# Performance work log

Hardware: AMD Instinct MI355X
Metric: run time of the kernel (lower is better)

## Reference

```python
import jax, jax.numpy as jnp
import numpy as np

B_SZ, L, D_INNER = 2, 1024, 2048
D_STATE, DT_RANK = 16, 64


def setup_inputs() -> dict:
    key = jax.random.key(0)
    k1, k2, k3, k4 = jax.random.split(key, 4)
    x = jax.random.normal(k1, (B_SZ, L, D_INNER), dtype=jnp.float32)
    # Linear weights: torch layout (out_features, in_features); scaled ~1/sqrt(fan_in)
    W_x = jax.random.normal(k2, (DT_RANK + 2 * D_STATE, D_INNER), dtype=jnp.float32) / np.sqrt(D_INNER)
    W_dt = jax.random.normal(k3, (D_INNER, DT_RANK), dtype=jnp.float32) / np.sqrt(DT_RANK)
    b_dt = jax.random.normal(k4, (D_INNER,), dtype=jnp.float32) * 0.1
    # A_log = log(arange(1, d_state+1)) broadcast to (d_inner, d_state), as in __init__
    A_log = jnp.broadcast_to(jnp.log(jnp.arange(1, D_STATE + 1, dtype=jnp.float32)), (D_INNER, D_STATE))
    D = jnp.ones((D_INNER,), dtype=jnp.float32)
    return {"x": x, "W_x": W_x, "W_dt": W_dt, "b_dt": b_dt, "A_log": A_log, "D": D}


def reference(x, W_x, W_dt, b_dt, A_log, D):
    # x: (B, L, d_inner)
    xz = jnp.einsum('bld,kd->blk', x, W_x)                       # (B, L, dt_rank + 2*d_state)
    delta_raw = xz[..., :DT_RANK]
    B_in = xz[..., DT_RANK:DT_RANK + D_STATE]                    # (B, L, d_state)
    C_in = xz[..., DT_RANK + D_STATE:]                           # (B, L, d_state)
    delta = jax.nn.softplus(jnp.einsum('blr,dr->bld', delta_raw, W_dt) + b_dt)  # (B, L, d_inner)
    A = -jnp.exp(A_log)                                          # (d_inner, d_state), negative
    A_bar = jnp.exp(delta[..., None] * A)                        # (B, L, d_inner, d_state)
    B_bar = delta[..., None] * B_in[:, :, None, :]               # (B, L, d_inner, d_state)

    def step(h, inputs):
        A_t, Bx_t, C_t = inputs                                  # (B,d,n), (B,d,n), (B,n)
        h = A_t * h + Bx_t
        y_t = jnp.sum(h * C_t[:, None, :], axis=-1)              # (B, d_inner)
        return h, y_t

    h0 = jnp.zeros((x.shape[0], D_INNER, D_STATE), dtype=x.dtype)
    Bx = B_bar * x[..., None]                                    # (B, L, d_inner, d_state)
    # scan over L: move L to leading axis
    _, ys = jax.lax.scan(step, h0, (jnp.moveaxis(A_bar, 1, 0), jnp.moveaxis(Bx, 1, 0), jnp.moveaxis(C_in, 1, 0)))
    y = jnp.moveaxis(ys, 0, 1) + D * x                           # (B, L, d_inner)
    return y
```

## Files before the change

kernel.cpp:

```cpp
#include <hip/hip_runtime.h>
#include <hip/hip_bf16.h>

#define B_SZ 2
#define LSEQ 1024
#define DIN  2048
#define DST  16
#define DTR  64
#define KTOT 96
#define NROW (B_SZ * LSEQ)
#define NCH  64
#define TCH  16
#define KSP  32

__device__ __forceinline__ float b2f(unsigned int u) {
    union { unsigned int i; float f; } v;
    v.i = (u & 0xffffu) << 16;
    return v.f;
}

__device__ __forceinline__ float ldf(const void* p, size_t i, bool f32) {
    return f32 ? ((const float*)p)[i] : b2f(((const unsigned short*)p)[i]);
}

__device__ __forceinline__ float4 ld4(const void* p, size_t i, bool f32) {
    if (f32) return *(const float4*)((const float*)p + i);
    const uint2 u = *(const uint2*)((const unsigned short*)p + i);
    float4 v;
    v.x = b2f(u.x); v.y = b2f(u.x >> 16);
    v.z = b2f(u.y); v.w = b2f(u.y >> 16);
    return v;
}

__device__ __forceinline__ float softplus_f(float v) {
    return (v > 20.f) ? v : log1pf(__expf(v));
}

__global__ __launch_bounds__(256) void k_detect(const void* __restrict__ x,
                                                int* __restrict__ flag) {
    __shared__ int cnt;
    if (threadIdx.x == 0) cnt = 0;
    __syncthreads();
    const unsigned short* u = (const unsigned short*)x;
    int my = 0;
    for (int i = threadIdx.x; i < 4096; i += 256) {
        unsigned short v = u[2 * i];
        float af = fabsf(b2f(v));
        if (v == 0 || (af >= 6.0e-8f && af <= 1.7e7f)) my++;
    }
    atomicAdd(&cnt, my);
    __syncthreads();
    if (threadIdx.x == 0) *flag = (cnt < 2048) ? 1 : 0;
}

__global__ __launch_bounds__(256, 4) void k_proj(
    const void* __restrict__ x,
    const void* __restrict__ Wx,
    const int*  __restrict__ flag,
    float* __restrict__ part)
{
    const bool f32 = (*flag != 0);
    __shared__ float lx[32][68];
    __shared__ float lw[32][100];
    const int tid = threadIdx.x;
    const int bx = blockIdx.x;
    const int by = blockIdx.y;
    const int rt = tid >> 4, ct = tid & 15;
    const int r0 = rt * 4, c0 = ct * 6;

    float acc[4][6];
    #pragma unroll
    for (int i = 0; i < 4; i++)
        #pragma unroll
        for (int k = 0; k < 6; k++) acc[i][k] = 0.f;

    for (int half = 0; half < 2; half++) {
        const int k0 = by * 64 + half * 32;
        #pragma unroll
        for (int it = 0; it < 2; it++) {
            const int idx = tid + it * 256;
            const int r = idx >> 3, q = idx & 7;
            float4 v = ld4(x, (size_t)(bx * 64 + r) * DIN + k0 + q * 4, f32);
            lx[q * 4 + 0][r] = v.x; lx[q * 4 + 1][r] = v.y;
            lx[q * 4 + 2][r] = v.z; lx[q * 4 + 3][r] = v.w;
        }
        #pragma unroll
        for (int it = 0; it < 3; it++) {
            const int idx = tid + it * 256;
            const int c = idx >> 3, q = idx & 7;
            float4 v = ld4(Wx, (size_t)c * DIN + k0 + q * 4, f32);
            lw[q * 4 + 0][c] = v.x; lw[q * 4 + 1][c] = v.y;
            lw[q * 4 + 2][c] = v.z; lw[q * 4 + 3][c] = v.w;
        }
        __syncthreads();

        #pragma unroll 4
        for (int j = 0; j < 32; j++) {
            const float4 xa = *(const float4*)&lx[j][r0];
            const float2 w0 = *(const float2*)&lw[j][c0];
            const float2 w1 = *(const float2*)&lw[j][c0 + 2];
            const float2 w2 = *(const float2*)&lw[j][c0 + 4];
            const float xr[4] = {xa.x, xa.y, xa.z, xa.w};
            const float wc[6] = {w0.x, w0.y, w1.x, w1.y, w2.x, w2.y};
            #pragma unroll
            for (int i = 0; i < 4; i++)
                #pragma unroll
                for (int k = 0; k < 6; k++)
                    acc[i][k] += xr[i] * wc[k];
        }
        __syncthreads();
    }

    float* p = part + ((size_t)by * NROW + bx * 64 + r0) * KTOT + c0;
    #pragma unroll
    for (int i = 0; i < 4; i++) {
        float* row = p + (size_t)i * KTOT;
        *(float2*)(row)     = make_float2(acc[i][0], acc[i][1]);
        *(float2*)(row + 2) = make_float2(acc[i][2], acc[i][3]);
        *(float2*)(row + 4) = make_float2(acc[i][4], acc[i][5]);
    }
}

__global__ __launch_bounds__(256, 4) void k_comb(
    const float* __restrict__ part,
    float* __restrict__ drw, float* __restrict__ Bin, float* __restrict__ Cin)
{
    const int idx = blockIdx.x * 256 + threadIdx.x;
    float s = 0.f;
    #pragma unroll 8
    for (int ks = 0; ks < KSP; ks++)
        s += part[(size_t)ks * NROW * KTOT + idx];
    const int r = idx / KTOT, c = idx % KTOT;
    if (c < DTR)            drw[r * DTR + c] = s;
    else if (c < DTR + DST) Bin[r * DST + (c - DTR)] = s;
    else                    Cin[r * DST + (c - DTR - DST)] = s;
}

__global__ __launch_bounds__(256, 2) void k_scan1(
    const void* __restrict__ x,
    const float* __restrict__ drw,
    const float* __restrict__ Bin,
    const void* __restrict__ Wdt,
    const void* __restrict__ bdt,
    const void* __restrict__ Alog,
    const int*  __restrict__ flag,
    float* __restrict__ Pb,
    float* __restrict__ Hb)
{
    const bool f32 = (*flag != 0);
    __shared__ float x_lds[TCH][256];
    __shared__ float dt_lds[TCH][256];
    __shared__ float drw_lds[TCH][DTR];
    __shared__ float Bs[TCH * DST];
    const int tid = threadIdx.x;
    const int d = blockIdx.x * 256 + tid;
    const int c = blockIdx.y;
    const int b = blockIdx.z;
    const int row0 = b * LSEQ + c * TCH;

    #pragma unroll
    for (int it = 0; it < 4; it++) {
        const int f4 = tid + it * 256;
        const int t  = f4 >> 6, q4 = f4 & 63;
        float4 v = ld4(x, (size_t)(row0 + t) * DIN + blockIdx.x * 256 + q4 * 4, f32);
        *(float4*)&x_lds[t][q4 * 4] = v;
    }
    #pragma unroll
    for (int it = 0; it < 4; it++) {
        const int f = tid + it * 256;
        const int r = f >> 6, k = f & 63;
        drw_lds[r][k] = drw[(size_t)(row0 + r) * DTR + k];
    }
    Bs[tid] = Bin[(size_t)row0 * DST + tid];

    float A[DST];
    #pragma unroll
    for (int sq = 0; sq < DST / 4; sq++) {
        float4 av = ld4(Alog, (size_t)d * DST + sq * 4, f32);
        A[sq * 4 + 0] = -__expf(av.x); A[sq * 4 + 1] = -__expf(av.y);
        A[sq * 4 + 2] = -__expf(av.z); A[sq * 4 + 3] = -__expf(av.w);
    }
    __syncthreads();

    {
        float dtv[TCH];
        const float bd = ldf(bdt, (size_t)d, f32);
        #pragma unroll
        for (int r = 0; r < TCH; r++) dtv[r] = bd;
        #pragma unroll 4
        for (int kq = 0; kq < DTR / 4; kq++) {
            const float4 w = ld4(Wdt, (size_t)d * DTR + kq * 4, f32);
            #pragma unroll
            for (int r = 0; r < TCH; r++) {
                const float4 a = *(const float4*)&drw_lds[r][kq * 4];
                dtv[r] += a.x * w.x; dtv[r] += a.y * w.y;
                dtv[r] += a.z * w.z; dtv[r] += a.w * w.w;
            }
        }
        #pragma unroll
        for (int r = 0; r < TCH; r++) dt_lds[r][tid] = softplus_f(dtv[r]);
    }

    float P[DST], H[DST];
    #pragma unroll
    for (int s = 0; s < DST; s++) { P[s] = 1.f; H[s] = 0.f; }

    #pragma unroll 1
    for (int t = 0; t < TCH; t++) {
        const float dtv_t = dt_lds[t][tid];
        const float xv    = x_lds[t][tid];
        const float u     = dtv_t * xv;
        const float* bs = Bs + t * DST;
        #pragma unroll
        for (int s = 0; s < DST; s++) {
            const float e = __expf(dtv_t * A[s]);
            P[s] *= e;
            H[s] = e * H[s] + u * bs[s];
        }
    }

    const size_t base = (size_t)(b * NCH + c) * DST * DIN + d;
    #pragma unroll
    for (int s = 0; s < DST; s++) {
        Pb[base + (size_t)s * DIN] = P[s];
        Hb[base + (size_t)s * DIN] = H[s];
    }
}

__global__ __launch_bounds__(256, 4) void k_scan2(
    const float* __restrict__ Pb,
    const float* __restrict__ Hb,
    float* __restrict__ hin)
{
    const int idx = blockIdx.x * 256 + threadIdx.x;
    const int b   = idx / (DST * DIN);
    const int rem = idx % (DST * DIN);
    float h = 0.f;
    #pragma unroll 4
    for (int c = 0; c < NCH; c++) {
        const size_t o = (size_t)(b * NCH + c) * DST * DIN + rem;
        const float p = Pb[o], hb = Hb[o];
        hin[o] = h;
        h = hb + p * h;
    }
}

__global__ __launch_bounds__(256, 2) void k_scan3(
    const void* __restrict__ x,
    const float* __restrict__ drw,
    const float* __restrict__ Bin,
    const float* __restrict__ Cin,
    const void* __restrict__ Wdt,
    const void* __restrict__ bdt,
    const void* __restrict__ Alog,
    const void* __restrict__ Dv,
    const float* __restrict__ hin,
    const int*  __restrict__ flag,
    void* __restrict__ y)
{
    const bool f32 = (*flag != 0);
    __shared__ float x_lds[TCH][256];
    __shared__ float dt_lds[TCH][256];
    __shared__ float drw_lds[TCH][DTR];
    __shared__ float Bs[TCH * DST];
    __shared__ float Cs[TCH * DST];
    const int tid = threadIdx.x;
    const int d = blockIdx.x * 256 + tid;
    const int c = blockIdx.y;
    const int b = blockIdx.z;
    const int row0 = b * LSEQ + c * TCH;

    #pragma unroll
    for (int it = 0; it < 4; it++) {
        const int f4 = tid + it * 256;
        const int t  = f4 >> 6, q4 = f4 & 63;
        float4 v = ld4(x, (size_t)(row0 + t) * DIN + blockIdx.x * 256 + q4 * 4, f32);
        *(float4*)&x_lds[t][q4 * 4] = v;
    }
    #pragma unroll
    for (int it = 0; it < 4; it++) {
        const int f = tid + it * 256;
        const int r = f >> 6, k = f & 63;
        drw_lds[r][k] = drw[(size_t)(row0 + r) * DTR + k];
    }
    Bs[tid] = Bin[(size_t)row0 * DST + tid];
    Cs[tid] = Cin[(size_t)row0 * DST + tid];

    float A[DST];
    #pragma unroll
    for (int sq = 0; sq < DST / 4; sq++) {
        float4 av = ld4(Alog, (size_t)d * DST + sq * 4, f32);
        A[sq * 4 + 0] = -__expf(av.x); A[sq * 4 + 1] = -__expf(av.y);
        A[sq * 4 + 2] = -__expf(av.z); A[sq * 4 + 3] = -__expf(av.w);
    }
    const float Dd = ldf(Dv, (size_t)d, f32);
    __syncthreads();

    {
        float dtv[TCH];
        const float bd = ldf(bdt, (size_t)d, f32);
        #pragma unroll
        for (int r = 0; r < TCH; r++) dtv[r] = bd;
        #pragma unroll 4
        for (int kq = 0; kq < DTR / 4; kq++) {
            const float4 w = ld4(Wdt, (size_t)d * DTR + kq * 4, f32);
            #pragma unroll
            for (int r = 0; r < TCH; r++) {
                const float4 a = *(const float4*)&drw_lds[r][kq * 4];
                dtv[r] += a.x * w.x; dtv[r] += a.y * w.y;
                dtv[r] += a.z * w.z; dtv[r] += a.w * w.w;
            }
        }
        #pragma unroll
        for (int r = 0; r < TCH; r++) dt_lds[r][tid] = softplus_f(dtv[r]);
    }

    float h[DST];
    const size_t base = (size_t)(b * NCH + c) * DST * DIN + d;
    #pragma unroll
    for (int s = 0; s < DST; s++) h[s] = hin[base + (size_t)s * DIN];

    #pragma unroll 1
    for (int t = 0; t < TCH; t++) {
        const float dtv_t = dt_lds[t][tid];
        const float xv    = x_lds[t][tid];
        const float u     = dtv_t * xv;
        const float* bs = Bs + t * DST;
        const float* cs = Cs + t * DST;
        float yv = Dd * xv;
        #pragma unroll
        for (int s = 0; s < DST; s++) {
            const float e = __expf(dtv_t * A[s]);
            h[s] = e * h[s] + u * bs[s];
            yv += h[s] * cs[s];
        }
        const size_t off = (size_t)(row0 + t) * DIN + d;
        if (f32) ((float*)y)[off] = yv;
        else     ((__hip_bfloat16*)y)[off] = __float2bfloat16(yv);
    }
}

extern "C" void kernel_launch(void* const* d_in, const int* in_sizes, int n_in,
                              void* d_out, int out_size, void* d_ws, size_t ws_size,
                              hipStream_t stream) {
    const void* x    = d_in[0];
    const void* Wx   = d_in[1];
    const void* Wdt  = d_in[2];
    const void* bdt  = d_in[3];
    const void* Alog = d_in[4];
    const void* Dv   = d_in[5];

    int*   flag  = (int*)d_ws;
    float* basep = (float*)d_ws + 16;
    float* drw   = basep;
    float* Bin   = drw + (size_t)NROW * DTR;
    float* Cin   = Bin + (size_t)NROW * DST;
    float* part  = Cin + (size_t)NROW * DST;
    float* Pb    = part + (size_t)KSP * NROW * KTOT;
    float* Hb    = Pb + (size_t)B_SZ * NCH * DST * DIN;
    float* hin   = Hb + (size_t)B_SZ * NCH * DST * DIN;

    k_detect<<<1, 256, 0, stream>>>(x, flag);

    k_proj<<<dim3(NROW / 64, KSP), 256, 0, stream>>>(x, Wx, flag, part);

    k_comb<<<(NROW * KTOT) / 256, 256, 0, stream>>>(part, drw, Bin, Cin);

    dim3 g1(DIN / 256, NCH, B_SZ);
    k_scan1<<<g1, 256, 0, stream>>>(x, drw, Bin, Wdt, bdt, Alog, flag, Pb, Hb);

    k_scan2<<<(B_SZ * DST * DIN) / 256, 256, 0, stream>>>(Pb, Hb, hin);

    k_scan3<<<g1, 256, 0, stream>>>(x, drw, Bin, Cin, Wdt, bdt, Alog, Dv, hin, flag, d_out);
}
```

Baseline: 208.1 us.

## Precompute softplus delta in a dedicated tiled GEMM kernel shared by both scan passes

Adds a k_dtg kernel that computes delta = softplus(delta_raw·W_dtᵀ + b) once as a tiled 64x64 GEMM and writes it to a workspace buffer. Both scan kernels previously recomputed this 64-deep dot product per element, so each now just loads the precomputed values. Chunk decay products are taken as exp(A·Σdt) rather than a running product, and B/C are interleaved into one buffer so each step does a single float2 LDS read. The cost is an extra launch plus an 8 MB delta write and two reads of it.

```diff
diff --git a/kernel.cpp b/kernel.cpp
--- a/kernel.cpp
+++ b/kernel.cpp
@@ -122,7 +122,7 @@
 
 __global__ __launch_bounds__(256, 4) void k_comb(
     const float* __restrict__ part,
-    float* __restrict__ drw, float* __restrict__ Bin, float* __restrict__ Cin)
+    float* __restrict__ drw, float* __restrict__ Bin, float* __restrict__ BC)
 {
     const int idx = blockIdx.x * 256 + threadIdx.x;
     float s = 0.f;
@@ -130,17 +130,86 @@
     for (int ks = 0; ks < KSP; ks++)
         s += part[(size_t)ks * NROW * KTOT + idx];
     const int r = idx / KTOT, c = idx % KTOT;
-    if (c < DTR)            drw[r * DTR + c] = s;
-    else if (c < DTR + DST) Bin[r * DST + (c - DTR)] = s;
-    else                    Cin[r * DST + (c - DTR - DST)] = s;
+    if (c < DTR) {
+        drw[r * DTR + c] = s;
+    } else if (c < DTR + DST) {
+        Bin[r * DST + (c - DTR)] = s;
+        BC[(size_t)r * 2 * DST + (c - DTR) * 2] = s;
+    } else {
+        BC[(size_t)r * 2 * DST + (c - DTR - DST) * 2 + 1] = s;
+    }
+}
+
+__global__ __launch_bounds__(256, 4) void k_dtg(
+    const float* __restrict__ drw,
+    const void* __restrict__ Wdt,
+    const void* __restrict__ bdt,
+    const int*  __restrict__ flag,
+    float* __restrict__ dt)
+{
+    const bool f32 = (*flag != 0);
+    __shared__ float la[DTR][65];
+    __shared__ float lb[DTR][65];
+    const int tid = threadIdx.x;
+    const int r0g = blockIdx.x * 64, c0g = blockIdx.y * 64;
+
+    #pragma unroll
+    for (int it = 0; it < 4; it++) {
+        const int idx = tid + it * 256;
+        const int r = idx >> 4, q = idx & 15;
+        const float4 v = *(const float4*)(drw + (size_t)(r0g + r) * DTR + q * 4);
+        la[q * 4 + 0][r] = v.x; la[q * 4 + 1][r] = v.y;
+        la[q * 4 + 2][r] = v.z; la[q * 4 + 3][r] = v.w;
+    }
+    #pragma unroll
+    for (int it = 0; it < 4; it++) {
+        const int idx = tid + it * 256;
+        const int c = idx >> 4, q = idx & 15;
+        const float4 v = ld4(Wdt, (size_t)(c0g + c) * DTR + q * 4, f32);
+        lb[q * 4 + 0][c] = v.x; lb[q * 4 + 1][c] = v.y;
+        lb[q * 4 + 2][c] = v.z; lb[q * 4 + 3][c] = v.w;
+    }
+    __syncthreads();
+
+    const int rt = tid >> 4, ct = tid & 15;
+    const int r0 = rt * 4, c0 = ct * 4;
+    float acc[4][4];
+    #pragma unroll
+    for (int i = 0; i < 4; i++)
+        #pragma unroll
+        for (int k = 0; k < 4; k++) acc[i][k] = 0.f;
+
+    #pragma unroll 4
+    for (int k = 0; k < DTR; k++) {
+        const float4 a = *(const float4*)&la[k][r0];
+        const float4 bq = *(const float4*)&lb[k][c0];
+        const float ar[4] = {a.x, a.y, a.z, a.w};
+        const float bc[4] = {bq.x, bq.y, bq.z, bq.w};
+        #pragma unroll
+        for (int i = 0; i < 4; i++)
+            #pragma unroll
+            for (int j = 0; j < 4; j++)
+                acc[i][j] += ar[i] * bc[j];
+    }
+
+    float bd[4];
+    #pragma unroll
+    for (int j = 0; j < 4; j++) bd[j] = ldf(bdt, (size_t)(c0g + c0 + j), f32);
+    #pragma unroll
+    for (int i = 0; i < 4; i++) {
+        float4 o;
+        o.x = softplus_f(acc[i][0] + bd[0]);
+        o.y = softplus_f(acc[i][1] + bd[1]);
+        o.z = softplus_f(acc[i][2] + bd[2]);
+        o.w = softplus_f(acc[i][3] + bd[3]);
+        *(float4*)(dt + (size_t)(r0g + r0 + i) * DIN + c0g + c0) = o;
+    }
 }
 
 __global__ __launch_bounds__(256, 2) void k_scan1(
     const void* __restrict__ x,
-    const float* __restrict__ drw,
+    const float* __restrict__ dtg,
     const float* __restrict__ Bin,
-    const void* __restrict__ Wdt,
-    const void* __restrict__ bdt,
     const void* __restrict__ Alog,
     const int*  __restrict__ flag,
     float* __restrict__ Pb,
@@ -149,7 +218,6 @@
     const bool f32 = (*flag != 0);
     __shared__ float x_lds[TCH][256];
     __shared__ float dt_lds[TCH][256];
-    __shared__ float drw_lds[TCH][DTR];
     __shared__ float Bs[TCH * DST];
     const int tid = threadIdx.x;
     const int d = blockIdx.x * 256 + tid;
@@ -163,12 +231,8 @@
         const int t  = f4 >> 6, q4 = f4 & 63;
         float4 v = ld4(x, (size_t)(row0 + t) * DIN + blockIdx.x * 256 + q4 * 4, f32);
         *(float4*)&x_lds[t][q4 * 4] = v;
-    }
-    #pragma unroll
-    for (int it = 0; it < 4; it++) {
-        const int f = tid + it * 256;
-        const int r = f >> 6, k = f & 63;
-        drw_lds[r][k] = drw[(size_t)(row0 + r) * DTR + k];
+        float4 w = *(const float4*)(dtg + (size_t)(row0 + t) * DIN + blockIdx.x * 256 + q4 * 4);
+        *(float4*)&dt_lds[t][q4 * 4] = w;
     }
     Bs[tid] = Bin[(size_t)row0 * DST + tid];
 
@@ -181,39 +245,21 @@
     }
     __syncthreads();
 
-    {
-        float dtv[TCH];
-        const float bd = ldf(bdt, (size_t)d, f32);
-        #pragma unroll
-        for (int r = 0; r < TCH; r++) dtv[r] = bd;
-        #pragma unroll 4
-        for (int kq = 0; kq < DTR / 4; kq++) {
-            const float4 w = ld4(Wdt, (size_t)d * DTR + kq * 4, f32);
-            #pragma unroll
-            for (int r = 0; r < TCH; r++) {
-                const float4 a = *(const float4*)&drw_lds[r][kq * 4];
-                dtv[r] += a.x * w.x; dtv[r] += a.y * w.y;
-                dtv[r] += a.z * w.z; dtv[r] += a.w * w.w;
-            }
-        }
-        #pragma unroll
-        for (int r = 0; r < TCH; r++) dt_lds[r][tid] = softplus_f(dtv[r]);
-    }
-
-    float P[DST], H[DST];
-    #pragma unroll
-    for (int s = 0; s < DST; s++) { P[s] = 1.f; H[s] = 0.f; }
+    float H[DST];
+    #pragma unroll
+    for (int s = 0; s < DST; s++) H[s] = 0.f;
+    float sdt = 0.f;
 
     #pragma unroll 1
     for (int t = 0; t < TCH; t++) {
         const float dtv_t = dt_lds[t][tid];
         const float xv    = x_lds[t][tid];
         const float u     = dtv_t * xv;
+        sdt += dtv_t;
         const float* bs = Bs + t * DST;
         #pragma unroll
         for (int s = 0; s < DST; s++) {
             const float e = __expf(dtv_t * A[s]);
-            P[s] *= e;
             H[s] = e * H[s] + u * bs[s];
         }
     }
@@ -221,7 +267,7 @@
     const size_t base = (size_t)(b * NCH + c) * DST * DIN + d;
     #pragma unroll
     for (int s = 0; s < DST; s++) {
-        Pb[base + (size_t)s * DIN] = P[s];
+        Pb[base + (size_t)s * DIN] = __expf(A[s] * sdt);
         Hb[base + (size_t)s * DIN] = H[s];
     }
 }
@@ -246,11 +292,8 @@
 
 __global__ __launch_bounds__(256, 2) void k_scan3(
     const void* __restrict__ x,
-    const float* __restrict__ drw,
-    const float* __restrict__ Bin,
-    const float* __restrict__ Cin,
-    const void* __restrict__ Wdt,
-    const void* __restrict__ bdt,
+    const float* __restrict__ dtg,
+    const float* __restrict__ BC,
     const void* __restrict__ Alog,
     const void* __restrict__ Dv,
     const float* __restrict__ hin,
@@ -260,9 +303,7 @@
     const bool f32 = (*flag != 0);
     __shared__ float x_lds[TCH][256];
     __shared__ float dt_lds[TCH][256];
-    __shared__ float drw_lds[TCH][DTR];
-    __shared__ float Bs[TCH * DST];
-    __shared__ float Cs[TCH * DST];
+    __shared__ float BCs[TCH * DST][2];
     const int tid = threadIdx.x;
     const int d = blockIdx.x * 256 + tid;
     const int c = blockIdx.y;
@@ -275,15 +316,10 @@
         const int t  = f4 >> 6, q4 = f4 & 63;
         float4 v = ld4(x, (size_t)(row0 + t) * DIN + blockIdx.x * 256 + q4 * 4, f32);
         *(float4*)&x_lds[t][q4 * 4] = v;
-    }
-    #pragma unroll
-    for (int it = 0; it < 4; it++) {
-        const int f = tid + it * 256;
-        const int r = f >> 6, k = f & 63;
-        drw_lds[r][k] = drw[(size_t)(row0 + r) * DTR + k];
-    }
-    Bs[tid] = Bin[(size_t)row0 * DST + tid];
-    Cs[tid] = Cin[(size_t)row0 * DST + tid];
+        float4 w = *(const float4*)(dtg + (size_t)(row0 + t) * DIN + blockIdx.x * 256 + q4 * 4);
+        *(float4*)&dt_lds[t][q4 * 4] = w;
+    }
+    *(float2*)&BCs[tid][0] = *(const float2*)(BC + (size_t)row0 * 2 * DST + tid * 2);
 
     float A[DST];
     #pragma unroll
@@ -293,45 +329,25 @@
         A[sq * 4 + 2] = -__expf(av.z); A[sq * 4 + 3] = -__expf(av.w);
     }
     const float Dd = ldf(Dv, (size_t)d, f32);
-    __syncthreads();
-
-    {
-        float dtv[TCH];
-        const float bd = ldf(bdt, (size_t)d, f32);
-        #pragma unroll
-        for (int r = 0; r < TCH; r++) dtv[r] = bd;
-        #pragma unroll 4
-        for (int kq = 0; kq < DTR / 4; kq++) {
-            const float4 w = ld4(Wdt, (size_t)d * DTR + kq * 4, f32);
-            #pragma unroll
-            for (int r = 0; r < TCH; r++) {
-                const float4 a = *(const float4*)&drw_lds[r][kq * 4];
-                dtv[r] += a.x * w.x; dtv[r] += a.y * w.y;
-                dtv[r] += a.z * w.z; dtv[r] += a.w * w.w;
-            }
-        }
-        #pragma unroll
-        for (int r = 0; r < TCH; r++) dt_lds[r][tid] = softplus_f(dtv[r]);
-    }
 
     float h[DST];
     const size_t base = (size_t)(b * NCH + c) * DST * DIN + d;
     #pragma unroll
     for (int s = 0; s < DST; s++) h[s] = hin[base + (size_t)s * DIN];
+    __syncthreads();
 
     #pragma unroll 1
     for (int t = 0; t < TCH; t++) {
         const float dtv_t = dt_lds[t][tid];
         const float xv    = x_lds[t][tid];
         const float u     = dtv_t * xv;
-        const float* bs = Bs + t * DST;
-        const float* cs = Cs + t * DST;
         float yv = Dd * xv;
         #pragma unroll
         for (int s = 0; s < DST; s++) {
+            const float2 bc = *(const float2*)&BCs[t * DST + s][0];
             const float e = __expf(dtv_t * A[s]);
-            h[s] = e * h[s] + u * bs[s];
-            yv += h[s] * cs[s];
+            h[s] = e * h[s] + u * bc.x;
+            yv += h[s] * bc.y;
         }
         const size_t off = (size_t)(row0 + t) * DIN + d;
         if (f32) ((float*)y)[off] = yv;
@@ -353,9 +369,10 @@
     float* basep = (float*)d_ws + 16;
     float* drw   = basep;
     float* Bin   = drw + (size_t)NROW * DTR;
-    float* Cin   = Bin + (size_t)NROW * DST;
-    float* part  = Cin + (size_t)NROW * DST;
-    float* Pb    = part + (size_t)KSP * NROW * KTOT;
+    float* BC    = Bin + (size_t)NROW * DST;
+    float* part  = BC + (size_t)NROW * DST * 2;
+    float* dtg   = part + (size_t)KSP * NROW * KTOT;
+    float* Pb    = dtg + (size_t)NROW * DIN;
     float* Hb    = Pb + (size_t)B_SZ * NCH * DST * DIN;
     float* hin   = Hb + (size_t)B_SZ * NCH * DST * DIN;
 
@@ -363,12 +380,14 @@
 
     k_proj<<<dim3(NROW / 64, KSP), 256, 0, stream>>>(x, Wx, flag, part);
 
-    k_comb<<<(NROW * KTOT) / 256, 256, 0, stream>>>(part, drw, Bin, Cin);
+    k_comb<<<(NROW * KTOT) / 256, 256, 0, stream>>>(part, drw, Bin, BC);
+
+    k_dtg<<<dim3(NROW / 64, DIN / 64), 256, 0, stream>>>(drw, Wdt, bdt, flag, dtg);
 
     dim3 g1(DIN / 256, NCH, B_SZ);
-    k_scan1<<<g1, 256, 0, stream>>>(x, drw, Bin, Wdt, bdt, Alog, flag, Pb, Hb);
+    k_scan1<<<g1, 256, 0, stream>>>(x, dtg, Bin, Alog, flag, Pb, Hb);
 
     k_scan2<<<(B_SZ * DST * DIN) / 256, 256, 0, stream>>>(Pb, Hb, hin);
 
-    k_scan3<<<g1, 256, 0, stream>>>(x, drw, Bin, Cin, Wdt, bdt, Alog, Dv, hin, flag, d_out);
-}
+    k_scan3<<<g1, 256, 0, stream>>>(x, dtg, BC, Alog, Dv, hin, flag, d_out);
+}
```

After: 183.9 us. -11.6%, faster.
